# Kernel optimization log

Hardware: AMD Instinct MI355X
Metric: run time of the kernel (lower is better)

The kernel has to match this reference:

```python
import jax, jax.numpy as jnp
import numpy as np

B, T, C, H, D, G, V, M = 4, 1024, 768, 12, 4, 4, 32000, 1024
S = C // H


def layernorm(x, g, b, eps=1e-5):
    mu = jnp.mean(x, -1, keepdims=True)
    var = jnp.mean(jnp.square(x - mu), -1, keepdims=True)
    return (x - mu) * jax.lax.rsqrt(var + eps) * g + b


def setup_inputs() -> dict:
    key = jax.random.key(0)
    ks = jax.random.split(key, 12)
    std = 0.02  # matches _init_weights normal(0, 0.02)
    n = lambda k, sh: jax.random.normal(k, sh, jnp.float32) * std
    return {
        'x': jax.random.randint(ks[0], (B, T), 0, V),
        'y': jax.random.randint(ks[1], (B, T), 0, V),
        'wordemb': n(ks[2], (V, C)),
        'posemb': n(ks[3], (M, C)),
        'Wq': n(ks[4], (D, C, C)),
        'Wk': n(ks[5], (D, C, C)),
        'Wv': n(ks[6], (D, C, C)),
        'Wo': n(ks[7], (D, C, C)),
        'bo': jnp.zeros((D, C), jnp.float32),
        'ln1_g': jnp.ones((D, C), jnp.float32),
        'ln1_b': jnp.zeros((D, C), jnp.float32),
        'W1': n(ks[8], (D, C, G * C)),
        'b1': jnp.zeros((D, G * C), jnp.float32),
        'W2': n(ks[9], (D, G * C, C)),
        'b2': jnp.zeros((D, C), jnp.float32),
        'ln2_g': jnp.ones((D, C), jnp.float32),
        'ln2_b': jnp.zeros((D, C), jnp.float32),
        'Wl': n(ks[10], (C, V)),
        'bl': jnp.zeros((V,), jnp.float32),
    }


def _forward(x, y, wordemb, posemb, Wq, Wk, Wv, Wo, bo, ln1_g, ln1_b,
             W1, b1, W2, b2, ln2_g, ln2_b, Wl, bl):
    b, t = x.shape
    emb = wordemb[x] + posemb[:t][None, :, :]  # (b,t,c)
    causal = jnp.tril(jnp.ones((t, t), bool))

    def block(h_in, p):
        wq, wk, wv, wo, bo_, g1, be1, w1, b1_, w2, b2_, g2, be2 = p
        q = (h_in @ wq).reshape(b, t, H, S)
        k = (h_in @ wk).reshape(b, t, H, S)
        v = (h_in @ wv).reshape(b, t, H, S)
        # note: original scales by sqrt(channels), NOT sqrt(head_dim)
        w = jnp.einsum('bqhs,bkhs->bhqk', q, k) / jnp.sqrt(jnp.float32(C))
        w = jnp.where(causal, w, -jnp.inf)
        w = jax.nn.softmax(w, axis=-1)
        att = jnp.einsum('bhqk,bkhs->bqhs', w, v).reshape(b, t, C)
        att = att @ wo + bo_
        h1 = h_in + layernorm(att, g1, be1)   # x + norm1(attn(x))
        ff = jax.nn.relu(h1 @ w1 + b1_) @ w2 + b2_
        h2 = h1 + layernorm(ff, g2, be2)      # x + norm2(ff(x)); dropout=0
        return h2, None

    hfin, _ = jax.lax.scan(
        block, emb,
        (Wq, Wk, Wv, Wo, bo, ln1_g, ln1_b, W1, b1, W2, b2, ln2_g, ln2_b))
    logits = hfin @ Wl + bl  # (b,t,v)
    logp = jax.nn.log_softmax(logits, axis=-1)
    nll = -jnp.take_along_axis(logp, y[..., None], axis=-1)[..., 0]
    loss = jnp.mean(nll)
    return logits, loss


def reference(x, y, wordemb, posemb, Wq, Wk, Wv, Wo, bo, ln1_g, ln1_b,
              W1, b1, W2, b2, ln2_g, ln2_b, Wl, bl):
    return _forward(x, y, wordemb, posemb, Wq, Wk, Wv, Wo, bo, ln1_g, ln1_b,
                    W1, b1, W2, b2, ln2_g, ln2_b, Wl, bl)
```

## Files before the change

kernel.cpp:

```cpp
#include <hip/hip_runtime.h>

#define Bn 4
#define Tn 1024
#define Cn 768
#define Hn 12
#define Dn 4
#define Vn 32000
#define BTn (Bn*Tn)
#define NBX 125

typedef __attribute__((ext_vector_type(8))) short short8;
typedef __attribute__((ext_vector_type(4))) float f32x4;

__device__ __forceinline__ unsigned short f2bf(float f) {
  union { float f; unsigned u; } v; v.f = f;
  unsigned r = v.u + 0x7fffu + ((v.u >> 16) & 1u);
  return (unsigned short)(r >> 16);
}

__device__ __forceinline__ void gload_lds16(const void* g, void* l) {
  __builtin_amdgcn_global_load_lds(
      (const __attribute__((address_space(1))) void*)g,
      (__attribute__((address_space(3))) void*)l, 16, 0, 0);
}

__global__ __launch_bounds__(256)
void transpose_bf16_kernel(const float* __restrict__ src, unsigned short* __restrict__ dst,
                           int K, int N) {
  __shared__ float tile[32][33];
  const int tx = threadIdx.x, ty = threadIdx.y;
  const int n0 = blockIdx.x * 32, k0 = blockIdx.y * 32;
#pragma unroll
  for (int i = 0; i < 4; ++i)
    tile[ty + i*8][tx] = src[(size_t)(k0 + ty + i*8) * N + n0 + tx];
  __syncthreads();
#pragma unroll
  for (int i = 0; i < 4; ++i)
    dst[(size_t)(n0 + ty + i*8) * K + k0 + tx] = f2bf(tile[tx][ty + i*8]);
}

__global__ __launch_bounds__(256)
void embed_kernel(const int* __restrict__ x, const float* __restrict__ wordemb,
                  const float* __restrict__ posemb, float* __restrict__ h,
                  unsigned short* __restrict__ hb) {
  int i4 = blockIdx.x * 256 + threadIdx.x;
  int row = i4 / (Cn/4), c4 = i4 % (Cn/4);
  int t = row & (Tn - 1);
  int tok = x[row];
  float4 a = ((const float4*)wordemb)[(size_t)tok * (Cn/4) + c4];
  float4 p = ((const float4*)posemb)[(size_t)t * (Cn/4) + c4];
  float4 s; s.x = a.x+p.x; s.y = a.y+p.y; s.z = a.z+p.z; s.w = a.w+p.w;
  ((float4*)h)[i4] = s;
  ushort4 u; u.x = f2bf(s.x); u.y = f2bf(s.y); u.z = f2bf(s.z); u.w = f2bf(s.w);
  ((ushort4*)hb)[i4] = u;
}

template<int WM, int WN, int MI, int NJ, int MINW>
__global__ __launch_bounds__(WM*WN*64, MINW)
void gemm_db(const unsigned short* __restrict__ A, const unsigned short* __restrict__ Bt,
             const float* __restrict__ bias, float* __restrict__ Cf,
             unsigned short* __restrict__ Cb, int M, int N, int K, int relu) {
  constexpr int BM = WM*MI*16, BN = WN*NJ*16, ROWS = BM + BN;
  __shared__ __align__(16) unsigned short lds[2*ROWS*32];
  const int tid = threadIdx.x;
  const int gx = gridDim.x;
  const int flat = blockIdx.x + gx*blockIdx.y;
  const int q = (gx * gridDim.y) >> 3;
  const int swz = (flat & 7)*q + (flat >> 3);
  const int by = swz % gx, bx = swz / gx;
  const int lane = tid & 63, w = tid >> 6;
  const int wr = w / WN, wc = w % WN;
  const int lr = lane & 15, lq = lane >> 4;
  const int xm = (lr >> 1) & 3;
  const int srow = lane >> 2, sslot = (lane & 3) ^ ((lane >> 3) & 3);
  const int NT = K >> 5;

  f32x4 acc[MI][NJ];
#pragma unroll
  for (int i = 0; i < MI; ++i)
#pragma unroll
    for (int j = 0; j < NJ; ++j)
      acc[i][j] = (f32x4){0.f, 0.f, 0.f, 0.f};

  const unsigned short* aS = A  + (size_t)(by*BM + w*32 + srow)*K + sslot*8;
  const unsigned short* bS = Bt + (size_t)(bx*BN + w*32 + srow)*K + sslot*8;

  auto STAGE = [&](int tile) {
    unsigned short* ba = &lds[(tile & 1)*ROWS*32];
    unsigned short* bb = ba + BM*32;
    const int k0 = tile*32;
    gload_lds16(aS + k0,                &ba[(w*32)*32]);
    gload_lds16(aS + k0 + (size_t)16*K, &ba[(w*32+16)*32]);
    gload_lds16(bS + k0,                &bb[(w*32)*32]);
    gload_lds16(bS + k0 + (size_t)16*K, &bb[(w*32+16)*32]);
  };

  STAGE(0);
  for (int t = 0; t < NT; ++t) {
    if (t + 1 < NT) {
      STAGE(t + 1);
      asm volatile("s_waitcnt vmcnt(4)" ::: "memory");
    } else {
      asm volatile("s_waitcnt vmcnt(0)" ::: "memory");
    }
    __builtin_amdgcn_s_barrier();
    __builtin_amdgcn_sched_barrier(0);
    const unsigned short* ba = &lds[(t & 1)*ROWS*32];
    const unsigned short* bb = ba + BM*32;
    short8 af[MI], bf[NJ];
#pragma unroll
    for (int i = 0; i < MI; ++i)
      af[i] = *(const short8*)&ba[(wr*MI*16 + i*16 + lr)*32 + (lq ^ xm)*8];
#pragma unroll
    for (int j = 0; j < NJ; ++j)
      bf[j] = *(const short8*)&bb[(wc*NJ*16 + j*16 + lr)*32 + (lq ^ xm)*8];
    __builtin_amdgcn_s_setprio(1);
#pragma unroll
    for (int i = 0; i < MI; ++i)
#pragma unroll
      for (int j = 0; j < NJ; ++j)
        acc[i][j] = __builtin_amdgcn_mfma_f32_16x16x32_bf16(af[i], bf[j], acc[i][j], 0, 0, 0);
    __builtin_amdgcn_s_setprio(0);
    __builtin_amdgcn_s_barrier();
  }

#pragma unroll
  for (int mi = 0; mi < MI; ++mi)
#pragma unroll
    for (int nj = 0; nj < NJ; ++nj)
#pragma unroll
      for (int r = 0; r < 4; ++r) {
        int grow = by*BM + wr*MI*16 + mi*16 + lq*4 + r;
        int gcol = bx*BN + wc*NJ*16 + nj*16 + lr;
        float v = acc[mi][nj][r];
        if (bias) v += bias[gcol];
        if (relu) v = fmaxf(v, 0.f);
        size_t idx = (size_t)grow * N + gcol;
        if (Cf) Cf[idx] = v;
        if (Cb) Cb[idx] = f2bf(v);
      }
}

__global__ __launch_bounds__(512, 2)
void gemm_vocab(const unsigned short* __restrict__ A, const unsigned short* __restrict__ Bt,
                const float* __restrict__ bias, float* __restrict__ Cf,
                float2* __restrict__ lsepart) {
  constexpr int MIH = 4, NJ = 4, BM = 256, ROWS = 512, K = 768, N = Vn, NT = 24;
  __shared__ __align__(16) unsigned short lds[4*ROWS*32];
  const int tid = threadIdx.x;
  const int bid = blockIdx.x;
  const int swz = (bid & 7)*250 + (bid >> 3);
  const int by = swz & 15, bx = swz >> 4;
  const int lane = tid & 63, w = tid >> 6;
  const int wr = w >> 2, wc = w & 3;
  const int lr = lane & 15, lq = lane >> 4;
  const int xm = (lr >> 1) & 3;
  const int srow = lane >> 2, sslot = (lane & 3) ^ ((lane >> 3) & 3);

  f32x4 accLo[MIH][NJ], accHi[MIH][NJ];
#pragma unroll
  for (int i = 0; i < MIH; ++i)
#pragma unroll
    for (int j = 0; j < NJ; ++j) {
      accLo[i][j] = (f32x4){0.f,0.f,0.f,0.f};
      accHi[i][j] = (f32x4){0.f,0.f,0.f,0.f};
    }

  const unsigned short* aS = A  + (size_t)(by*BM + w*32 + srow)*K + sslot*8;
  const unsigned short* bS = Bt + (size_t)(bx*256 + w*32 + srow)*K + sslot*8;

  auto stageA = [&](int tile) {
    unsigned short* ba = &lds[(tile & 3)*ROWS*32];
    const int k0 = tile*32;
    gload_lds16(aS + k0,                &ba[(w*32)*32]);
    gload_lds16(aS + k0 + (size_t)16*K, &ba[(w*32+16)*32]);
  };
  auto stageB = [&](int tile) {
    unsigned short* bb = &lds[(tile & 3)*ROWS*32 + BM*32];
    const int k0 = tile*32;
    gload_lds16(bS + k0,                &bb[(w*32)*32]);
    gload_lds16(bS + k0 + (size_t)16*K, &bb[(w*32+16)*32]);
  };

  short8 afLo[MIH], afHi[MIH], bf[NJ];
  auto rdALo = [&](int tile) {
    const unsigned short* ba = &lds[(tile & 3)*ROWS*32];
#pragma unroll
    for (int i = 0; i < MIH; ++i)
      afLo[i] = *(const short8*)&ba[(wr*128 + i*16 + lr)*32 + (lq ^ xm)*8];
  };
  auto rdAHi = [&](int tile) {
    const unsigned short* ba = &lds[(tile & 3)*ROWS*32];
#pragma unroll
    for (int i = 0; i < MIH; ++i)
      afHi[i] = *(const short8*)&ba[(wr*128 + (MIH+i)*16 + lr)*32 + (lq ^ xm)*8];
  };
  auto rdB = [&](int tile) {
    const unsigned short* bb = &lds[(tile & 3)*ROWS*32 + BM*32];
#pragma unroll
    for (int nj = 0; nj < NJ; ++nj)
      bf[nj] = *(const short8*)&bb[(wc*64 + nj*16 + lr)*32 + (lq ^ xm)*8];
  };
  auto clLo = [&]() {
    __builtin_amdgcn_s_setprio(1);
#pragma unroll
    for (int i = 0; i < MIH; ++i)
#pragma unroll
      for (int nj = 0; nj < NJ; ++nj)
        accLo[i][nj] = __builtin_amdgcn_mfma_f32_16x16x32_bf16(afLo[i], bf[nj], accLo[i][nj], 0, 0, 0);
    __builtin_amdgcn_s_setprio(0);
  };
  auto clHi = [&]() {
    __builtin_amdgcn_s_setprio(1);
#pragma unroll
    for (int i = 0; i < MIH; ++i)
#pragma unroll
      for (int nj = 0; nj < NJ; ++nj)
        accHi[i][nj] = __builtin_amdgcn_mfma_f32_16x16x32_bf16(afHi[i], bf[nj], accHi[i][nj], 0, 0, 0);
    __builtin_amdgcn_s_setprio(0);
  };

  stageA(0); stageB(0); stageA(1); stageB(1);
  asm volatile("s_waitcnt vmcnt(4)" ::: "memory");
  __builtin_amdgcn_s_barrier();
  __builtin_amdgcn_sched_barrier(0);

  for (int t = 0; t < NT; ++t) {
    rdALo(t); rdB(t);
    if (t + 2 < NT) stageA(t + 2);
    __builtin_amdgcn_s_barrier();
    __builtin_amdgcn_sched_barrier(0);
    clLo();
    __builtin_amdgcn_s_barrier();
    rdAHi(t);
    if (t + 2 < NT) stageB(t + 2);
    if (t + 2 < NT)      { asm volatile("s_waitcnt vmcnt(4)" ::: "memory"); }
    else if (t + 1 < NT) { asm volatile("s_waitcnt vmcnt(0)" ::: "memory"); }
    __builtin_amdgcn_s_barrier();
    __builtin_amdgcn_sched_barrier(0);
    clHi();
    __builtin_amdgcn_s_barrier();
  }

  float2* part = (float2*)lds;
#pragma unroll
  for (int half = 0; half < 2; ++half) {
#pragma unroll
    for (int mi = 0; mi < MIH; ++mi)
#pragma unroll
      for (int r = 0; r < 4; ++r) {
        float v[NJ]; float m = -3.0e38f;
#pragma unroll
        for (int nj = 0; nj < NJ; ++nj) {
          int gcol = bx*256 + wc*64 + nj*16 + lr;
          float val = (half ? accHi[mi][nj][r] : accLo[mi][nj][r]) + bias[gcol];
          v[nj] = val;
          m = fmaxf(m, val);
        }
        int prow = wr*128 + half*64 + mi*16 + lq*4 + r;
        int grow = by*256 + prow;
        float* crow = Cf + (size_t)grow * N + bx*256 + wc*64 + lr;
#pragma unroll
        for (int nj = 0; nj < NJ; ++nj) crow[nj*16] = v[nj];
        float s = 0.f;
#pragma unroll
        for (int nj = 0; nj < NJ; ++nj) s += __expf(v[nj] - m);
#pragma unroll
        for (int mask = 1; mask < 16; mask <<= 1) {
          float m2 = __shfl_xor(m, mask), s2 = __shfl_xor(s, mask);
          float mn = fmaxf(m, m2);
          s = s*__expf(m - mn) + s2*__expf(m2 - mn);
          m = mn;
        }
        if (lr == 0) part[prow*4 + wc] = make_float2(m, s);
      }
  }
  __syncthreads();
  if (tid < 256) {
    float2 p = part[tid*4];
    float m = p.x, s = p.y;
#pragma unroll
    for (int wcc = 1; wcc < 4; ++wcc) {
      float2 p2 = part[tid*4 + wcc];
      float mn = fmaxf(m, p2.x);
      s = s*__expf(m - mn) + p2.y*__expf(p2.x - mn);
      m = mn;
    }
    lsepart[(size_t)(by*256 + tid)*NBX + bx] = make_float2(m, s);
  }
}

__global__ __launch_bounds__(256)
void vT_kernel(const unsigned short* __restrict__ qkvb, unsigned short* __restrict__ vT) {
  const int tb = blockIdx.x, hh = blockIdx.y, b = blockIdx.z;
  const int t = threadIdx.x;
  __shared__ unsigned short tile[64][65];
  const int r = t >> 2, c = t & 3;
  const unsigned short* src = qkvb + (size_t)(b*Tn + tb*64 + r) * 2304 + 1536 + hh*64 + c*16;
  short8 v0 = *(const short8*)src;
  short8 v1 = *(const short8*)(src + 8);
#pragma unroll
  for (int j = 0; j < 8; ++j) { tile[r][c*16 + j] = (unsigned short)v0[j]; tile[r][c*16 + 8 + j] = (unsigned short)v1[j]; }
  __syncthreads();
  unsigned short o[16];
#pragma unroll
  for (int j = 0; j < 16; ++j) o[j] = tile[c*16 + j][r];
  unsigned short* dst = vT + ((size_t)((b*Hn + hh)*64 + r)) * Tn + tb*64 + c*16;
  *(ushort4*)(dst)      = *(ushort4*)&o[0];
  *(ushort4*)(dst + 4)  = *(ushort4*)&o[4];
  *(ushort4*)(dst + 8)  = *(ushort4*)&o[8];
  *(ushort4*)(dst + 12) = *(ushort4*)&o[12];
}

__global__ __launch_bounds__(256)
void attn_mfma_kernel(const unsigned short* __restrict__ qkvb,
                      const unsigned short* __restrict__ vT,
                      unsigned short* __restrict__ attb) {
  const int qb = blockIdx.x, hh = blockIdx.y, b = blockIdx.z;
  const int t = threadIdx.x;
  const int lane = t & 63, w = t >> 6;
  const int lr = lane & 15, lg = lane >> 4;
  const float scale = 0.03608439182435161f;

  __shared__ unsigned short Ks[64*64];
  __shared__ unsigned short Vs[64*64];
  __shared__ unsigned short Ps[4][16][72];

  const unsigned short* qsrc = qkvb + (size_t)(b*Tn + qb*64 + w*16 + lr)*2304 + hh*64 + lg*8;
  short8 qa0 = *(const short8*)(qsrc);
  short8 qa1 = *(const short8*)(qsrc + 32);

  f32x4 acc[4];
#pragma unroll
  for (int dt = 0; dt < 4; ++dt) acc[dt] = (f32x4){0.f,0.f,0.f,0.f};
  float m_run[4], l_run[4];
#pragma unroll
  for (int r = 0; r < 4; ++r) { m_run[r] = -1e30f; l_run[r] = 0.f; }

  const int sr = t >> 2, c2 = t & 3;

  for (int kvb = 0; kvb <= qb; ++kvb) {
    __syncthreads();
    {
      const unsigned short* ksrc = qkvb + (size_t)(b*Tn + kvb*64 + sr)*2304 + 768 + hh*64 + c2*16;
      short8 k0 = *(const short8*)ksrc;
      short8 k1 = *(const short8*)(ksrc + 8);
      const unsigned short* vsrc = vT + ((size_t)((b*Hn + hh)*64 + sr))*Tn + kvb*64 + c2*16;
      short8 vv0 = *(const short8*)vsrc;
      short8 vv1 = *(const short8*)(vsrc + 8);
      int s0 = (2*c2) ^ (sr & 7), s1 = (2*c2 + 1) ^ (sr & 7);
      *(short8*)&Ks[sr*64 + s0*8] = k0;
      *(short8*)&Ks[sr*64 + s1*8] = k1;
      *(short8*)&Vs[sr*64 + s0*8] = vv0;
      *(short8*)&Vs[sr*64 + s1*8] = vv1;
    }
    __syncthreads();

    f32x4 s[4];
#pragma unroll
    for (int kt = 0; kt < 4; ++kt) {
      int krow = kt*16 + lr;
      short8 kf0 = *(const short8*)&Ks[krow*64 + ((0 + lg) ^ (krow & 7))*8];
      short8 kf1 = *(const short8*)&Ks[krow*64 + ((4 + lg) ^ (krow & 7))*8];
      f32x4 a = (f32x4){0.f,0.f,0.f,0.f};
      a = __builtin_amdgcn_mfma_f32_16x16x32_bf16(qa0, kf0, a, 0, 0, 0);
      a = __builtin_amdgcn_mfma_f32_16x16x32_bf16(qa1, kf1, a, 0, 0, 0);
      s[kt] = a;
    }
    const bool diag = (kvb == qb);
#pragma unroll
    for (int kt = 0; kt < 4; ++kt)
#pragma unroll
      for (int r = 0; r < 4; ++r) {
        float v = s[kt][r] * scale;
        if (diag && (kt*16 + lr > w*16 + lg*4 + r)) v = -1e30f;
        s[kt][r] = v;
      }
#pragma unroll
    for (int r = 0; r < 4; ++r) {
      float m = fmaxf(fmaxf(s[0][r], s[1][r]), fmaxf(s[2][r], s[3][r]));
      m = fmaxf(m, __shfl_xor(m, 1));
      m = fmaxf(m, __shfl_xor(m, 2));
      m = fmaxf(m, __shfl_xor(m, 4));
      m = fmaxf(m, __shfl_xor(m, 8));
      float mn = fmaxf(m_run[r], m);
      float corr = __expf(m_run[r] - mn);
      m_run[r] = mn;
      float ps = 0.f;
#pragma unroll
      for (int kt = 0; kt < 4; ++kt) {
        float p = __expf(s[kt][r] - mn);
        s[kt][r] = p;
        ps += p;
      }
      ps += __shfl_xor(ps, 1);
      ps += __shfl_xor(ps, 2);
      ps += __shfl_xor(ps, 4);
      ps += __shfl_xor(ps, 8);
      l_run[r] = l_run[r] * corr + ps;
#pragma unroll
      for (int dt = 0; dt < 4; ++dt) acc[dt][r] *= corr;
    }
#pragma unroll
    for (int kt = 0; kt < 4; ++kt)
#pragma unroll
      for (int r = 0; r < 4; ++r)
        Ps[w][lg*4 + r][kt*16 + lr] = f2bf(s[kt][r]);
    short8 pa0 = *(const short8*)&Ps[w][lr][lg*8];
    short8 pa1 = *(const short8*)&Ps[w][lr][32 + lg*8];
#pragma unroll
    for (int dt = 0; dt < 4; ++dt) {
      int drow = dt*16 + lr;
      short8 vf0 = *(const short8*)&Vs[drow*64 + ((0 + lg) ^ (drow & 7))*8];
      short8 vf1 = *(const short8*)&Vs[drow*64 + ((4 + lg) ^ (drow & 7))*8];
      acc[dt] = __builtin_amdgcn_mfma_f32_16x16x32_bf16(pa0, vf0, acc[dt], 0, 0, 0);
      acc[dt] = __builtin_amdgcn_mfma_f32_16x16x32_bf16(pa1, vf1, acc[dt], 0, 0, 0);
    }
  }

  unsigned short* obase = attb + (size_t)(b*Tn + qb*64 + w*16)*768 + hh*64;
#pragma unroll
  for (int dt = 0; dt < 4; ++dt)
#pragma unroll
    for (int r = 0; r < 4; ++r) {
      float v = acc[dt][r] / l_run[r];
      obase[(size_t)(lg*4 + r)*768 + dt*16 + lr] = f2bf(v);
    }
}

__global__ __launch_bounds__(256)
void ln_res_kernel(const float* __restrict__ x, float* __restrict__ h,
                   unsigned short* __restrict__ hb, const float* __restrict__ g,
                   const float* __restrict__ bb) {
  const int row = blockIdx.x, tid = threadIdx.x;
  const float* xr = x + (size_t)row * Cn;
  float v[3], s1 = 0.f, s2 = 0.f;
#pragma unroll
  for (int j = 0; j < 3; ++j) { v[j] = xr[tid + j*256]; s1 += v[j]; s2 += v[j]*v[j]; }
  __shared__ float r1[256], r2[256];
  r1[tid] = s1; r2[tid] = s2;
  __syncthreads();
  for (int s = 128; s > 0; s >>= 1) {
    if (tid < s) { r1[tid] += r1[tid+s]; r2[tid] += r2[tid+s]; }
    __syncthreads();
  }
  float mu = r1[0] * (1.f/768.f);
  float var = r2[0] * (1.f/768.f) - mu*mu;
  float rs = rsqrtf(var + 1e-5f);
  float* hr = h + (size_t)row * Cn;
  unsigned short* hbr = hb + (size_t)row * Cn;
#pragma unroll
  for (int j = 0; j < 3; ++j) {
    int c = tid + j*256;
    float y = hr[c] + (v[j]-mu)*rs*g[c] + bb[c];
    hr[c] = y;
    hbr[c] = f2bf(y);
  }
}

__global__ __launch_bounds__(128)
void loss_part_kernel(const float2* __restrict__ part, const float* __restrict__ logits,
                      const int* __restrict__ y, float* __restrict__ loss_rows) {
  const int row = blockIdx.x, tid = threadIdx.x;
  float m = -3.0e38f, s = 0.f;
  if (tid < NBX) { float2 p = part[(size_t)row*NBX + tid]; m = p.x; s = p.y; }
#pragma unroll
  for (int mask = 1; mask < 64; mask <<= 1) {
    float m2 = __shfl_xor(m, mask), s2 = __shfl_xor(s, mask);
    float mn = fmaxf(m, m2);
    s = s*__expf(m - mn) + s2*__expf(m2 - mn);
    m = mn;
  }
  __shared__ float mw[2], sw[2];
  if ((tid & 63) == 0) { mw[tid >> 6] = m; sw[tid >> 6] = s; }
  __syncthreads();
  if (tid == 0) {
    float m2 = mw[1], s2 = sw[1];
    float mn = fmaxf(m, m2);
    s = s*__expf(m - mn) + s2*__expf(m2 - mn);
    loss_rows[row] = mn + __logf(s) - logits[(size_t)row*Vn + y[row]];
  }
}

__global__ __launch_bounds__(256)
void loss_reduce_kernel(const float* __restrict__ loss_rows, float* __restrict__ out) {
  const int tid = threadIdx.x;
  float s = 0.f;
  for (int j = 0; j < BTn/256; ++j) s += loss_rows[tid + j*256];
  __shared__ float red[256];
  red[tid] = s; __syncthreads();
  for (int st = 128; st > 0; st >>= 1) {
    if (tid < st) red[tid] += red[tid+st];
    __syncthreads();
  }
  if (tid == 0) out[0] = red[0] * (1.f/(float)BTn);
}

extern "C" void kernel_launch(void* const* d_in, const int* in_sizes, int n_in,
                              void* d_out, int out_size, void* d_ws, size_t ws_size,
                              hipStream_t stream) {
  const int*   x       = (const int*)  d_in[0];
  const int*   y       = (const int*)  d_in[1];
  const float* wordemb = (const float*)d_in[2];
  const float* posemb  = (const float*)d_in[3];
  const float* Wq      = (const float*)d_in[4];
  const float* Wk      = (const float*)d_in[5];
  const float* Wv      = (const float*)d_in[6];
  const float* Wo      = (const float*)d_in[7];
  const float* bo      = (const float*)d_in[8];
  const float* ln1_g   = (const float*)d_in[9];
  const float* ln1_b   = (const float*)d_in[10];
  const float* W1      = (const float*)d_in[11];
  const float* b1      = (const float*)d_in[12];
  const float* W2      = (const float*)d_in[13];
  const float* b2      = (const float*)d_in[14];
  const float* ln2_g   = (const float*)d_in[15];
  const float* ln2_b   = (const float*)d_in[16];
  const float* Wl      = (const float*)d_in[17];
  const float* bl      = (const float*)d_in[18];

  char* ws = (char*)d_ws;
  size_t off = 0;
  auto alloc = [&](size_t bytes) -> char* {
    char* p = ws + off;
    off += (bytes + 255) & ~(size_t)255;
    return p;
  };
  unsigned short* wqkvT = (unsigned short*)alloc((size_t)Dn*2304*768*2);
  unsigned short* woT   = (unsigned short*)alloc((size_t)Dn*768*768*2);
  unsigned short* w1T   = (unsigned short*)alloc((size_t)Dn*3072*768*2);
  unsigned short* w2T   = (unsigned short*)alloc((size_t)Dn*768*3072*2);
  unsigned short* wlT   = (unsigned short*)alloc((size_t)Vn*768*2);
  float*          h     = (float*)alloc((size_t)BTn*Cn*4);
  unsigned short* hb    = (unsigned short*)alloc((size_t)BTn*Cn*2);
  unsigned short* qkvb  = (unsigned short*)alloc((size_t)BTn*3072*2);
  unsigned short* vTb   = (unsigned short*)alloc((size_t)Bn*Hn*64*Tn*2);
  unsigned short* attb  = (unsigned short*)alloc((size_t)BTn*Cn*2);
  float*          tmp   = (float*)alloc((size_t)BTn*Cn*4);
  float*          loss_rows = (float*)alloc((size_t)BTn*4);
  float2*         lsepart   = (float2*)alloc((size_t)BTn*NBX*8);
  unsigned short* ff1b  = qkvb;

  dim3 tb(32, 8);
  for (int d = 0; d < Dn; ++d) {
    transpose_bf16_kernel<<<dim3(24,24), tb, 0, stream>>>(Wq + (size_t)d*Cn*Cn, wqkvT + (size_t)d*2304*768,            Cn, Cn);
    transpose_bf16_kernel<<<dim3(24,24), tb, 0, stream>>>(Wk + (size_t)d*Cn*Cn, wqkvT + (size_t)d*2304*768 + 768*768,  Cn, Cn);
    transpose_bf16_kernel<<<dim3(24,24), tb, 0, stream>>>(Wv + (size_t)d*Cn*Cn, wqkvT + (size_t)d*2304*768 + 1536*768, Cn, Cn);
    transpose_bf16_kernel<<<dim3(24,24), tb, 0, stream>>>(Wo + (size_t)d*Cn*Cn, woT + (size_t)d*768*768,  Cn, Cn);
    transpose_bf16_kernel<<<dim3(96,24), tb, 0, stream>>>(W1 + (size_t)d*768*3072, w1T + (size_t)d*3072*768, 768, 3072);
    transpose_bf16_kernel<<<dim3(24,96), tb, 0, stream>>>(W2 + (size_t)d*3072*768, w2T + (size_t)d*768*3072, 3072, 768);
  }
  transpose_bf16_kernel<<<dim3(1000,24), tb, 0, stream>>>(Wl, wlT, 768, Vn);

  embed_kernel<<<(BTn*Cn/4)/256, 256, 0, stream>>>(x, wordemb, posemb, h, hb);

  for (int d = 0; d < Dn; ++d) {
    gemm_db<2,2,4,4,3><<<dim3(BTn/128, 2304/128), 256, 0, stream>>>(
        hb, wqkvT + (size_t)d*2304*768, nullptr, nullptr, qkvb, BTn, 2304, 768, 0);
    vT_kernel<<<dim3(Tn/64, Hn, Bn), 256, 0, stream>>>(qkvb, vTb);
    attn_mfma_kernel<<<dim3(Tn/64, Hn, Bn), 256, 0, stream>>>(qkvb, vTb, attb);
    gemm_db<2,2,4,4,3><<<dim3(BTn/128, 768/128), 256, 0, stream>>>(
        attb, woT + (size_t)d*768*768, bo + (size_t)d*768, tmp, nullptr, BTn, 768, 768, 0);
    ln_res_kernel<<<BTn, 256, 0, stream>>>(tmp, h, hb, ln1_g + (size_t)d*768, ln1_b + (size_t)d*768);
    gemm_db<2,2,4,4,3><<<dim3(BTn/128, 3072/128), 256, 0, stream>>>(
        hb, w1T + (size_t)d*3072*768, b1 + (size_t)d*3072, nullptr, ff1b, BTn, 3072, 768, 1);
    gemm_db<2,2,4,4,3><<<dim3(BTn/128, 768/128), 256, 0, stream>>>(
        ff1b, w2T + (size_t)d*768*3072, b2 + (size_t)d*768, tmp, nullptr, BTn, 768, 3072, 0);
    ln_res_kernel<<<BTn, 256, 0, stream>>>(tmp, h, hb, ln2_g + (size_t)d*768, ln2_b + (size_t)d*768);
  }

  float* logits = (float*)d_out;
  gemm_vocab<<<2000, 512, 0, stream>>>(hb, wlT, bl, logits, lsepart);
  loss_part_kernel<<<BTn, 128, 0, stream>>>(lsepart, logits, y, loss_rows);
  loss_reduce_kernel<<<1, 256, 0, stream>>>(loss_rows, logits + (size_t)BTn*Vn);
}
```

Baseline: 1.377 ms.

## Deepen GEMM K-tiles to 64 and interleave staging with split MFMA phases

The layer GEMM and vocab GEMM now load 64-wide K tiles as two 32-wide halves into double-buffered LDS. Global-to-LDS staging of the next tiles is interleaved between MFMA phases, which halves the number of main-loop iterations and barrier rounds per K. The vocab kernel uses larger LDS and drops to one block per CU, trading occupancy for deeper per-block prefetch. Weight transposes are batched over layers via blockIdx.z to cut launch count.

```diff
diff --git a/kernel.cpp b/kernel.cpp
--- a/kernel.cpp
+++ b/kernel.cpp
@@ -25,8 +25,10 @@
 }
 
 __global__ __launch_bounds__(256)
-void transpose_bf16_kernel(const float* __restrict__ src, unsigned short* __restrict__ dst,
-                           int K, int N) {
+void transpose_bf16_kernel(const float* __restrict__ src0, unsigned short* __restrict__ dst0,
+                           int K, int N, size_t sStride, size_t dStride) {
+  const float* src = src0 + blockIdx.z * sStride;
+  unsigned short* dst = dst0 + blockIdx.z * dStride;
   __shared__ float tile[32][33];
   const int tx = threadIdx.x, ty = threadIdx.y;
   const int n0 = blockIdx.x * 32, k0 = blockIdx.y * 32;
@@ -55,83 +57,106 @@
   ((ushort4*)hb)[i4] = u;
 }
 
-template<int WM, int WN, int MI, int NJ, int MINW>
-__global__ __launch_bounds__(WM*WN*64, MINW)
-void gemm_db(const unsigned short* __restrict__ A, const unsigned short* __restrict__ Bt,
-             const float* __restrict__ bias, float* __restrict__ Cf,
-             unsigned short* __restrict__ Cb, int M, int N, int K, int relu) {
-  constexpr int BM = WM*MI*16, BN = WN*NJ*16, ROWS = BM + BN;
-  __shared__ __align__(16) unsigned short lds[2*ROWS*32];
+__global__ __launch_bounds__(256, 2)
+void gemm_l(const unsigned short* __restrict__ A, const unsigned short* __restrict__ Bt,
+            const float* __restrict__ bias, float* __restrict__ Cf,
+            unsigned short* __restrict__ Cb, int M, int N, int K, int relu) {
+  __shared__ __align__(16) unsigned short lds[2*16384];
   const int tid = threadIdx.x;
   const int gx = gridDim.x;
   const int flat = blockIdx.x + gx*blockIdx.y;
-  const int q = (gx * gridDim.y) >> 3;
-  const int swz = (flat & 7)*q + (flat >> 3);
+  const int chq = (gx * gridDim.y) >> 3;
+  const int swz = (flat & 7)*chq + (flat >> 3);
   const int by = swz % gx, bx = swz / gx;
   const int lane = tid & 63, w = tid >> 6;
-  const int wr = w / WN, wc = w % WN;
+  const int wr = w >> 1, wc = w & 1;
   const int lr = lane & 15, lq = lane >> 4;
   const int xm = (lr >> 1) & 3;
-  const int srow = lane >> 2, sslot = (lane & 3) ^ ((lane >> 3) & 3);
-  const int NT = K >> 5;
-
-  f32x4 acc[MI][NJ];
-#pragma unroll
-  for (int i = 0; i < MI; ++i)
-#pragma unroll
-    for (int j = 0; j < NJ; ++j)
+  const int sslot = (lane & 3) ^ ((lane >> 3) & 3);
+  const int NT = K >> 6;
+
+  f32x4 acc[4][4];
+#pragma unroll
+  for (int i = 0; i < 4; ++i)
+#pragma unroll
+    for (int j = 0; j < 4; ++j)
       acc[i][j] = (f32x4){0.f, 0.f, 0.f, 0.f};
 
-  const unsigned short* aS = A  + (size_t)(by*BM + w*32 + srow)*K + sslot*8;
-  const unsigned short* bS = Bt + (size_t)(bx*BN + w*32 + srow)*K + sslot*8;
-
-  auto STAGE = [&](int tile) {
-    unsigned short* ba = &lds[(tile & 1)*ROWS*32];
-    unsigned short* bb = ba + BM*32;
-    const int k0 = tile*32;
-    gload_lds16(aS + k0,                &ba[(w*32)*32]);
-    gload_lds16(aS + k0 + (size_t)16*K, &ba[(w*32+16)*32]);
-    gload_lds16(bS + k0,                &bb[(w*32)*32]);
-    gload_lds16(bS + k0 + (size_t)16*K, &bb[(w*32+16)*32]);
-  };
-
-  STAGE(0);
+  const unsigned short* aS = A  + (size_t)(by*128 + w*16 + (lane>>2))*K + sslot*8;
+  const unsigned short* bS = Bt + (size_t)(bx*128 + w*16 + (lane>>2))*K + sslot*8;
+
+  auto stA = [&](int t) {
+    unsigned short* d = &lds[(t&1)*16384];
+    const int k0 = t*64;
+#pragma unroll
+    for (int kh = 0; kh < 2; ++kh)
+#pragma unroll
+      for (int i = 0; i < 2; ++i)
+        gload_lds16(aS + k0 + kh*32 + (size_t)i*64*K, d + kh*4096 + (i*64 + w*16)*32);
+  };
+  auto stB = [&](int t) {
+    unsigned short* d = &lds[(t&1)*16384 + 8192];
+    const int k0 = t*64;
+#pragma unroll
+    for (int kh = 0; kh < 2; ++kh)
+#pragma unroll
+      for (int i = 0; i < 2; ++i)
+        gload_lds16(bS + k0 + kh*32 + (size_t)i*64*K, d + kh*4096 + (i*64 + w*16)*32);
+  };
+  auto rdA = [&](int t, int kh, short8* af) {
+    const unsigned short* p = &lds[(t&1)*16384 + kh*4096];
+#pragma unroll
+    for (int mi = 0; mi < 4; ++mi)
+      af[mi] = *(const short8*)&p[(wr*64 + mi*16 + lr)*32 + (lq ^ xm)*8];
+  };
+  auto rdB = [&](int t, int kh, short8* bf) {
+    const unsigned short* p = &lds[(t&1)*16384 + 8192 + kh*4096];
+#pragma unroll
+    for (int nj = 0; nj < 4; ++nj)
+      bf[nj] = *(const short8*)&p[(wc*64 + nj*16 + lr)*32 + (lq ^ xm)*8];
+  };
+
+  short8 af0[4], af1[4], bf0[4], bf1[4];
+  stA(0); stB(0); stA(1);
+
   for (int t = 0; t < NT; ++t) {
-    if (t + 1 < NT) {
-      STAGE(t + 1);
-      asm volatile("s_waitcnt vmcnt(4)" ::: "memory");
-    } else {
-      asm volatile("s_waitcnt vmcnt(0)" ::: "memory");
-    }
-    __builtin_amdgcn_s_barrier();
-    __builtin_amdgcn_sched_barrier(0);
-    const unsigned short* ba = &lds[(t & 1)*ROWS*32];
-    const unsigned short* bb = ba + BM*32;
-    short8 af[MI], bf[NJ];
-#pragma unroll
-    for (int i = 0; i < MI; ++i)
-      af[i] = *(const short8*)&ba[(wr*MI*16 + i*16 + lr)*32 + (lq ^ xm)*8];
-#pragma unroll
-    for (int j = 0; j < NJ; ++j)
-      bf[j] = *(const short8*)&bb[(wc*NJ*16 + j*16 + lr)*32 + (lq ^ xm)*8];
+    if (t + 1 < NT) { asm volatile("s_waitcnt vmcnt(4)" ::: "memory"); }
+    else            { asm volatile("s_waitcnt vmcnt(0)" ::: "memory"); }
+    __builtin_amdgcn_s_barrier();
+    __builtin_amdgcn_sched_barrier(0);
+    rdA(t, 0, af0); rdA(t, 1, af1); rdB(t, 0, bf0);
+    if (t + 1 < NT) stB(t + 1);
+    __builtin_amdgcn_s_barrier();
+    __builtin_amdgcn_sched_barrier(0);
     __builtin_amdgcn_s_setprio(1);
 #pragma unroll
-    for (int i = 0; i < MI; ++i)
-#pragma unroll
-      for (int j = 0; j < NJ; ++j)
-        acc[i][j] = __builtin_amdgcn_mfma_f32_16x16x32_bf16(af[i], bf[j], acc[i][j], 0, 0, 0);
+    for (int i = 0; i < 4; ++i)
+#pragma unroll
+      for (int j = 0; j < 4; ++j)
+        acc[i][j] = __builtin_amdgcn_mfma_f32_16x16x32_bf16(af0[i], bf0[j], acc[i][j], 0, 0, 0);
     __builtin_amdgcn_s_setprio(0);
     __builtin_amdgcn_s_barrier();
-  }
-
-#pragma unroll
-  for (int mi = 0; mi < MI; ++mi)
-#pragma unroll
-    for (int nj = 0; nj < NJ; ++nj)
+    rdB(t, 1, bf1);
+    if (t + 2 < NT) stA(t + 2);
+    __builtin_amdgcn_s_barrier();
+    __builtin_amdgcn_sched_barrier(0);
+    __builtin_amdgcn_s_setprio(1);
+#pragma unroll
+    for (int i = 0; i < 4; ++i)
+#pragma unroll
+      for (int j = 0; j < 4; ++j)
+        acc[i][j] = __builtin_amdgcn_mfma_f32_16x16x32_bf16(af1[i], bf1[j], acc[i][j], 0, 0, 0);
+    __builtin_amdgcn_s_setprio(0);
+  }
+
+#pragma unroll
+  for (int mi = 0; mi < 4; ++mi)
+#pragma unroll
+    for (int nj = 0; nj < 4; ++nj)
 #pragma unroll
       for (int r = 0; r < 4; ++r) {
-        int grow = by*BM + wr*MI*16 + mi*16 + lq*4 + r;
-        int gcol = bx*BN + wc*NJ*16 + nj*16 + lr;
+        int grow = by*128 + wr*64 + mi*16 + lq*4 + r;
+        int gcol = bx*128 + wc*64 + nj*16 + lr;
         float v = acc[mi][nj][r];
         if (bias) v += bias[gcol];
         if (relu) v = fmaxf(v, 0.f);
@@ -141,12 +166,12 @@
       }
 }
 
-__global__ __launch_bounds__(512, 2)
+__global__ __launch_bounds__(512, 1)
 void gemm_vocab(const unsigned short* __restrict__ A, const unsigned short* __restrict__ Bt,
                 const float* __restrict__ bias, float* __restrict__ Cf,
                 float2* __restrict__ lsepart) {
-  constexpr int MIH = 4, NJ = 4, BM = 256, ROWS = 512, K = 768, N = Vn, NT = 24;
-  __shared__ __align__(16) unsigned short lds[4*ROWS*32];
+  constexpr int K = 768, N = Vn, NT = 12;
+  __shared__ __align__(16) unsigned short lds[2*32768];
   const int tid = threadIdx.x;
   const int bid = blockIdx.x;
   const int swz = (bid & 7)*250 + (bid >> 3);
@@ -155,103 +180,115 @@
   const int wr = w >> 2, wc = w & 3;
   const int lr = lane & 15, lq = lane >> 4;
   const int xm = (lr >> 1) & 3;
-  const int srow = lane >> 2, sslot = (lane & 3) ^ ((lane >> 3) & 3);
-
-  f32x4 accLo[MIH][NJ], accHi[MIH][NJ];
-#pragma unroll
-  for (int i = 0; i < MIH; ++i)
-#pragma unroll
-    for (int j = 0; j < NJ; ++j) {
+  const int sslot = (lane & 3) ^ ((lane >> 3) & 3);
+
+  f32x4 accLo[4][4], accHi[4][4];
+#pragma unroll
+  for (int i = 0; i < 4; ++i)
+#pragma unroll
+    for (int j = 0; j < 4; ++j) {
       accLo[i][j] = (f32x4){0.f,0.f,0.f,0.f};
       accHi[i][j] = (f32x4){0.f,0.f,0.f,0.f};
     }
 
-  const unsigned short* aS = A  + (size_t)(by*BM + w*32 + srow)*K + sslot*8;
-  const unsigned short* bS = Bt + (size_t)(bx*256 + w*32 + srow)*K + sslot*8;
-
-  auto stageA = [&](int tile) {
-    unsigned short* ba = &lds[(tile & 3)*ROWS*32];
-    const int k0 = tile*32;
-    gload_lds16(aS + k0,                &ba[(w*32)*32]);
-    gload_lds16(aS + k0 + (size_t)16*K, &ba[(w*32+16)*32]);
-  };
-  auto stageB = [&](int tile) {
-    unsigned short* bb = &lds[(tile & 3)*ROWS*32 + BM*32];
-    const int k0 = tile*32;
-    gload_lds16(bS + k0,                &bb[(w*32)*32]);
-    gload_lds16(bS + k0 + (size_t)16*K, &bb[(w*32+16)*32]);
-  };
-
-  short8 afLo[MIH], afHi[MIH], bf[NJ];
-  auto rdALo = [&](int tile) {
-    const unsigned short* ba = &lds[(tile & 3)*ROWS*32];
-#pragma unroll
-    for (int i = 0; i < MIH; ++i)
-      afLo[i] = *(const short8*)&ba[(wr*128 + i*16 + lr)*32 + (lq ^ xm)*8];
-  };
-  auto rdAHi = [&](int tile) {
-    const unsigned short* ba = &lds[(tile & 3)*ROWS*32];
-#pragma unroll
-    for (int i = 0; i < MIH; ++i)
-      afHi[i] = *(const short8*)&ba[(wr*128 + (MIH+i)*16 + lr)*32 + (lq ^ xm)*8];
-  };
-  auto rdB = [&](int tile) {
-    const unsigned short* bb = &lds[(tile & 3)*ROWS*32 + BM*32];
-#pragma unroll
-    for (int nj = 0; nj < NJ; ++nj)
-      bf[nj] = *(const short8*)&bb[(wc*64 + nj*16 + lr)*32 + (lq ^ xm)*8];
-  };
-  auto clLo = [&]() {
+  const unsigned short* aS = A  + (size_t)(by*256 + w*16 + (lane>>2))*K + sslot*8;
+  const unsigned short* bS = Bt + (size_t)(bx*256 + w*16 + (lane>>2))*K + sslot*8;
+
+  auto stA = [&](int t) {
+    unsigned short* d = &lds[(t&1)*32768];
+    const int k0 = t*64;
+#pragma unroll
+    for (int kh = 0; kh < 2; ++kh)
+#pragma unroll
+      for (int i = 0; i < 2; ++i)
+        gload_lds16(aS + k0 + kh*32 + (size_t)i*128*K, d + kh*8192 + (i*128 + w*16)*32);
+  };
+  auto stB = [&](int t) {
+    unsigned short* d = &lds[(t&1)*32768 + 16384];
+    const int k0 = t*64;
+#pragma unroll
+    for (int kh = 0; kh < 2; ++kh)
+#pragma unroll
+      for (int i = 0; i < 2; ++i)
+        gload_lds16(bS + k0 + kh*32 + (size_t)i*128*K, d + kh*8192 + (i*128 + w*16)*32);
+  };
+  auto rdA = [&](int t, int kh, int mh, short8* af) {
+    const unsigned short* p = &lds[(t&1)*32768 + kh*8192];
+#pragma unroll
+    for (int mi = 0; mi < 4; ++mi)
+      af[mi] = *(const short8*)&p[(wr*128 + mh*64 + mi*16 + lr)*32 + (lq ^ xm)*8];
+  };
+  auto rdB = [&](int t, int kh, short8* bf) {
+    const unsigned short* p = &lds[(t&1)*32768 + 16384 + kh*8192];
+#pragma unroll
+    for (int nj = 0; nj < 4; ++nj)
+      bf[nj] = *(const short8*)&p[(wc*64 + nj*16 + lr)*32 + (lq ^ xm)*8];
+  };
+
+  short8 aLo0[4], aHi0[4], aLo1[4], aHi1[4], bf0[4], bf1[4];
+  stA(0); stB(0); stA(1); stB(1);
+
+  for (int t = 0; t < NT; ++t) {
+    if (t + 1 < NT) { asm volatile("s_waitcnt vmcnt(8)" ::: "memory"); }
+    else            { asm volatile("s_waitcnt vmcnt(0)" ::: "memory"); }
+    __builtin_amdgcn_s_barrier();
+    __builtin_amdgcn_sched_barrier(0);
+    rdA(t, 0, 0, aLo0); rdA(t, 0, 1, aHi0); rdB(t, 0, bf0);
+    __builtin_amdgcn_s_barrier();
+    __builtin_amdgcn_sched_barrier(0);
     __builtin_amdgcn_s_setprio(1);
 #pragma unroll
-    for (int i = 0; i < MIH; ++i)
-#pragma unroll
-      for (int nj = 0; nj < NJ; ++nj)
-        accLo[i][nj] = __builtin_amdgcn_mfma_f32_16x16x32_bf16(afLo[i], bf[nj], accLo[i][nj], 0, 0, 0);
+    for (int i = 0; i < 4; ++i)
+#pragma unroll
+      for (int j = 0; j < 4; ++j)
+        accLo[i][j] = __builtin_amdgcn_mfma_f32_16x16x32_bf16(aLo0[i], bf0[j], accLo[i][j], 0, 0, 0);
     __builtin_amdgcn_s_setprio(0);
-  };
-  auto clHi = [&]() {
+    __builtin_amdgcn_s_barrier();
+    rdA(t, 1, 0, aLo1); rdA(t, 1, 1, aHi1);
+    __builtin_amdgcn_s_barrier();
+    __builtin_amdgcn_sched_barrier(0);
     __builtin_amdgcn_s_setprio(1);
 #pragma unroll
-    for (int i = 0; i < MIH; ++i)
-#pragma unroll
-      for (int nj = 0; nj < NJ; ++nj)
-        accHi[i][nj] = __builtin_amdgcn_mfma_f32_16x16x32_bf16(afHi[i], bf[nj], accHi[i][nj], 0, 0, 0);
+    for (int i = 0; i < 4; ++i)
+#pragma unroll
+      for (int j = 0; j < 4; ++j)
+        accHi[i][j] = __builtin_amdgcn_mfma_f32_16x16x32_bf16(aHi0[i], bf0[j], accHi[i][j], 0, 0, 0);
     __builtin_amdgcn_s_setprio(0);
-  };
-
-  stageA(0); stageB(0); stageA(1); stageB(1);
-  asm volatile("s_waitcnt vmcnt(4)" ::: "memory");
-  __builtin_amdgcn_s_barrier();
-  __builtin_amdgcn_sched_barrier(0);
-
-  for (int t = 0; t < NT; ++t) {
-    rdALo(t); rdB(t);
-    if (t + 2 < NT) stageA(t + 2);
-    __builtin_amdgcn_s_barrier();
-    __builtin_amdgcn_sched_barrier(0);
-    clLo();
-    __builtin_amdgcn_s_barrier();
-    rdAHi(t);
-    if (t + 2 < NT) stageB(t + 2);
-    if (t + 2 < NT)      { asm volatile("s_waitcnt vmcnt(4)" ::: "memory"); }
-    else if (t + 1 < NT) { asm volatile("s_waitcnt vmcnt(0)" ::: "memory"); }
-    __builtin_amdgcn_s_barrier();
-    __builtin_amdgcn_sched_barrier(0);
-    clHi();
-    __builtin_amdgcn_s_barrier();
+    __builtin_amdgcn_s_barrier();
+    rdB(t, 1, bf1);
+    if (t + 2 < NT) stA(t + 2);
+    __builtin_amdgcn_s_barrier();
+    __builtin_amdgcn_sched_barrier(0);
+    __builtin_amdgcn_s_setprio(1);
+#pragma unroll
+    for (int i = 0; i < 4; ++i)
+#pragma unroll
+      for (int j = 0; j < 4; ++j)
+        accLo[i][j] = __builtin_amdgcn_mfma_f32_16x16x32_bf16(aLo1[i], bf1[j], accLo[i][j], 0, 0, 0);
+    __builtin_amdgcn_s_setprio(0);
+    __builtin_amdgcn_s_barrier();
+    if (t + 2 < NT) stB(t + 2);
+    __builtin_amdgcn_s_barrier();
+    __builtin_amdgcn_sched_barrier(0);
+    __builtin_amdgcn_s_setprio(1);
+#pragma unroll
+    for (int i = 0; i < 4; ++i)
+#pragma unroll
+      for (int j = 0; j < 4; ++j)
+        accHi[i][j] = __builtin_amdgcn_mfma_f32_16x16x32_bf16(aHi1[i], bf1[j], accHi[i][j], 0, 0, 0);
+    __builtin_amdgcn_s_setprio(0);
   }
 
   float2* part = (float2*)lds;
 #pragma unroll
   for (int half = 0; half < 2; ++half) {
 #pragma unroll
-    for (int mi = 0; mi < MIH; ++mi)
+    for (int mi = 0; mi < 4; ++mi)
 #pragma unroll
       for (int r = 0; r < 4; ++r) {
-        float v[NJ]; float m = -3.0e38f;
-#pragma unroll
-        for (int nj = 0; nj < NJ; ++nj) {
+        float v[4]; float m = -3.0e38f;
+#pragma unroll
+        for (int nj = 0; nj < 4; ++nj) {
           int gcol = bx*256 + wc*64 + nj*16 + lr;
           float val = (half ? accHi[mi][nj][r] : accLo[mi][nj][r]) + bias[gcol];
           v[nj] = val;
@@ -261,10 +298,10 @@
         int grow = by*256 + prow;
         float* crow = Cf + (size_t)grow * N + bx*256 + wc*64 + lr;
 #pragma unroll
-        for (int nj = 0; nj < NJ; ++nj) crow[nj*16] = v[nj];
+        for (int nj = 0; nj < 4; ++nj) crow[nj*16] = v[nj];
         float s = 0.f;
 #pragma unroll
-        for (int nj = 0; nj < NJ; ++nj) s += __expf(v[nj] - m);
+        for (int nj = 0; nj < 4; ++nj) s += __expf(v[nj] - m);
 #pragma unroll
         for (int mask = 1; mask < 16; mask <<= 1) {
           float m2 = __shfl_xor(m, mask), s2 = __shfl_xor(s, mask);
@@ -542,29 +579,27 @@
   unsigned short* ff1b  = qkvb;
 
   dim3 tb(32, 8);
+  transpose_bf16_kernel<<<dim3(24,24,Dn), tb, 0, stream>>>(Wq, wqkvT,             Cn, Cn, (size_t)Cn*Cn, (size_t)2304*768);
+  transpose_bf16_kernel<<<dim3(24,24,Dn), tb, 0, stream>>>(Wk, wqkvT + 768*768,   Cn, Cn, (size_t)Cn*Cn, (size_t)2304*768);
+  transpose_bf16_kernel<<<dim3(24,24,Dn), tb, 0, stream>>>(Wv, wqkvT + 1536*768,  Cn, Cn, (size_t)Cn*Cn, (size_t)2304*768);
+  transpose_bf16_kernel<<<dim3(24,24,Dn), tb, 0, stream>>>(Wo, woT,               Cn, Cn, (size_t)Cn*Cn, (size_t)768*768);
+  transpose_bf16_kernel<<<dim3(96,24,Dn), tb, 0, stream>>>(W1, w1T, 768, 3072, (size_t)768*3072, (size_t)3072*768);
+  transpose_bf16_kernel<<<dim3(24,96,Dn), tb, 0, stream>>>(W2, w2T, 3072, 768, (size_t)3072*768, (size_t)768*3072);
+  transpose_bf16_kernel<<<dim3(1000,24,1), tb, 0, stream>>>(Wl, wlT, 768, Vn, 0, 0);
+
+  embed_kernel<<<(BTn*Cn/4)/256, 256, 0, stream>>>(x, wordemb, posemb, h, hb);
+
   for (int d = 0; d < Dn; ++d) {
-    transpose_bf16_kernel<<<dim3(24,24), tb, 0, stream>>>(Wq + (size_t)d*Cn*Cn, wqkvT + (size_t)d*2304*768,            Cn, Cn);
-    transpose_bf16_kernel<<<dim3(24,24), tb, 0, stream>>>(Wk + (size_t)d*Cn*Cn, wqkvT + (size_t)d*2304*768 + 768*768,  Cn, Cn);
-    transpose_bf16_kernel<<<dim3(24,24), tb, 0, stream>>>(Wv + (size_t)d*Cn*Cn, wqkvT + (size_t)d*2304*768 + 1536*768, Cn, Cn);
-    transpose_bf16_kernel<<<dim3(24,24), tb, 0, stream>>>(Wo + (size_t)d*Cn*Cn, woT + (size_t)d*768*768,  Cn, Cn);
-    transpose_bf16_kernel<<<dim3(96,24), tb, 0, stream>>>(W1 + (size_t)d*768*3072, w1T + (size_t)d*3072*768, 768, 3072);
-    transpose_bf16_kernel<<<dim3(24,96), tb, 0, stream>>>(W2 + (size_t)d*3072*768, w2T + (size_t)d*768*3072, 3072, 768);
-  }
-  transpose_bf16_kernel<<<dim3(1000,24), tb, 0, stream>>>(Wl, wlT, 768, Vn);
-
-  embed_kernel<<<(BTn*Cn/4)/256, 256, 0, stream>>>(x, wordemb, posemb, h, hb);
-
-  for (int d = 0; d < Dn; ++d) {
-    gemm_db<2,2,4,4,3><<<dim3(BTn/128, 2304/128), 256, 0, stream>>>(
+    gemm_l<<<dim3(BTn/128, 2304/128), 256, 0, stream>>>(
         hb, wqkvT + (size_t)d*2304*768, nullptr, nullptr, qkvb, BTn, 2304, 768, 0);
     vT_kernel<<<dim3(Tn/64, Hn, Bn), 256, 0, stream>>>(qkvb, vTb);
     attn_mfma_kernel<<<dim3(Tn/64, Hn, Bn), 256, 0, stream>>>(qkvb, vTb, attb);
-    gemm_db<2,2,4,4,3><<<dim3(BTn/128, 768/128), 256, 0, stream>>>(
+    gemm_l<<<dim3(BTn/128, 768/128), 256, 0, stream>>>(
         attb, woT + (size_t)d*768*768, bo + (size_t)d*768, tmp, nullptr, BTn, 768, 768, 0);
     ln_res_kernel<<<BTn, 256, 0, stream>>>(tmp, h, hb, ln1_g + (size_t)d*768, ln1_b + (size_t)d*768);
-    gemm_db<2,2,4,4,3><<<dim3(BTn/128, 3072/128), 256, 0, stream>>>(
+    gemm_l<<<dim3(BTn/128, 3072/128), 256, 0, stream>>>(
         hb, w1T + (size_t)d*3072*768, b1 + (size_t)d*3072, nullptr, ff1b, BTn, 3072, 768, 1);
-    gemm_db<2,2,4,4,3><<<dim3(BTn/128, 768/128), 256, 0, stream>>>(
+    gemm_l<<<dim3(BTn/128, 768/128), 256, 0, stream>>>(
         ff1b, w2T + (size_t)d*768*3072, b2 + (size_t)d*768, tmp, nullptr, BTn, 768, 3072, 0);
     ln_res_kernel<<<BTn, 256, 0, stream>>>(tmp, h, hb, ln2_g + (size_t)d*768, ln2_b + (size_t)d*768);
   }
```

After: 1.334 ms. -3.1%, faster.
